# Optimization experiments

Hardware: AMD Instinct MI355X
Metric: run time of the kernel (lower is better)

## Reference

```python
import jax, jax.numpy as jnp
import numpy as np
from jax import lax

B, S, H, V, J, K = 8, 512, 768, 35004, 30, 9
PAD = 0

def setup_inputs() -> dict:
    key = jax.random.key(0)
    ks = jax.random.split(key, 12)
    std = 0.02
    return {
        'x': jax.random.randint(ks[0], (B, S), 0, V),
        'decoder_input': jax.random.normal(ks[1], (B, J, H), jnp.float32),
        'encoder_output': jax.random.normal(ks[2], (B, S, H), jnp.float32),
        'hidden': jax.random.normal(ks[3], (1, B, H), jnp.float32),
        'teacher': jax.random.randint(ks[4], (B, J, K), 0, V),
        'max_len': K,
        'embed': jax.random.normal(ks[5], (V, H), jnp.float32) * std,
        'w_ih': jax.random.normal(ks[6], (3 * H, H), jnp.float32) * std,
        'w_hh': jax.random.normal(ks[7], (3 * H, H), jnp.float32) * std,
        'b_ih': jnp.zeros((3 * H,), jnp.float32),
        'b_hh': jnp.zeros((3 * H,), jnp.float32),
        'wg_w': jax.random.normal(ks[8], (1, 3 * H), jnp.float32) * std,
        'wg_b': jnp.zeros((1,), jnp.float32),
    }

def gru_cell(w, h, w_ih, w_hh, b_ih, b_hh):
    # PyTorch GRU gate order: reset, update, new
    gi = w @ w_ih.T + b_ih          # [B,3H]
    gh = h @ w_hh.T + b_hh          # [B,3H]
    ir, iz, inn = jnp.split(gi, 3, axis=-1)
    hr, hz, hn = jnp.split(gh, 3, axis=-1)
    r = jax.nn.sigmoid(ir + hr)
    z = jax.nn.sigmoid(iz + hz)
    n = jnp.tanh(inn + r * hn)
    return (1.0 - z) * n + z * h

def reference(x, decoder_input, encoder_output, hidden, teacher, max_len,
              embed, w_ih, w_hh, b_ih, b_hh, wg_w, wg_b):
    mask = (x == PAD)                      # [B,S]
    batch_ix = jnp.arange(x.shape[0])[:, None]

    def tok_step(carry, teach_t):
        w, h = carry                       # w,h: [B,H]; teach_t: [B]
        h = gru_cell(w, h, w_ih, w_hh, b_ih, b_hh)
        logits_hist = jnp.einsum('bsh,bh->bs', encoder_output, h)
        logits_hist = jnp.where(mask, -1e9, logits_hist)
        a_hist = jax.nn.softmax(logits_hist, axis=-1)          # [B,S]
        a_vocab = jax.nn.softmax(h @ embed.T, axis=-1)         # [B,V]
        context = jnp.einsum('bs,bsh->bh', a_hist, encoder_output)
        p_gen = jax.nn.sigmoid(
            jnp.concatenate([w, h, context], axis=-1) @ wg_w.T + wg_b)  # [B,1]
        p_ctx = jnp.zeros_like(a_vocab).at[batch_ix, x].add(a_hist)     # scatter_add pointer copy
        p_final = p_gen * a_vocab + (1.0 - p_gen) * p_ctx
        w_next = embed[teach_t]            # teacher forcing (dropout omitted: eval mode)
        return (w_next, h), p_final

    def slot_step(h, slot_in):
        w0, teach_j = slot_in              # w0: [B,H]; teach_j: [K,B]
        (_, h), p = lax.scan(tok_step, (w0, h), teach_j)
        return h, p                        # p: [K,B,V]

    h0 = hidden[0]                                      # [B,H]
    slots = jnp.swapaxes(decoder_input, 0, 1)           # [J,B,H]
    teach = jnp.transpose(teacher, (1, 2, 0))           # [J,K,B]
    _, outs = lax.scan(slot_step, h0, (slots, teach))   # [J,K,B,V]
    return jnp.transpose(outs, (2, 0, 1, 3))            # [B,J,K,V]
```

## Files before the change

kernel.cpp:

```cpp
#include <hip/hip_runtime.h>
#include <hip/hip_bf16.h>

typedef _Float16 f16;
typedef _Float16 f16x8 __attribute__((ext_vector_type(8)));
typedef _Float16 h2 __attribute__((ext_vector_type(2)));
typedef float f32x4 __attribute__((ext_vector_type(4)));
typedef unsigned ui4v __attribute__((ext_vector_type(4)));
typedef unsigned long long ull;

#define B_ 8
#define S_ 512
#define H_ 768
#define V_ 35004
#define J_ 30
#define K_ 9
#define R_ 2160
#define H3 2304
#define CBLK 24
#define CUPB 32
#define VMT 17
#define VNT 274


__global__ void k_zero(int* p, int n) {
    int i = blockIdx.x * 256 + threadIdx.x;
    if (i < n) p[i] = 0;
}

__global__ void k_cast(const float* __restrict__ s, f16* __restrict__ d, long n) {
    for (long i = (long)blockIdx.x * 256 + threadIdx.x; i < n; i += (long)gridDim.x * 256)
        d[i] = (f16)s[i];
}

__global__ void k_build_wall(const float* __restrict__ emb, const float* __restrict__ dec,
                             const int* __restrict__ teacher, f16* __restrict__ Wall) {
    int r = blockIdx.x;
    int b = r / 270, s = r % 270, j = s / 9, t = s % 9;
    const float* src = (t == 0) ? dec + ((long)b * J_ + j) * H_
                                : emb + (long)teacher[((long)b * J_ + j) * K_ + (t - 1)] * H_;
    f16* dst = Wall + (long)r * H_;
    for (int c = threadIdx.x; c < H_; c += 256) dst[c] = (f16)src[c];
}

__global__ void k_build_enc(const float* __restrict__ enc, f16* __restrict__ ehi,
                            f16* __restrict__ elo, f16* __restrict__ encT) {
    long n = (long)B_ * S_ * H_;
    for (long i = (long)blockIdx.x * 256 + threadIdx.x; i < n; i += (long)gridDim.x * 256) {
        float v = enc[i];
        f16 hi = (f16)v;
        ehi[i] = hi;
        elo[i] = (f16)(v - (float)hi);
        int h = (int)(i % H_);
        long bs = i / H_;
        int s = (int)(bs % S_), b = (int)(bs / S_);
        encT[((long)b * H_ + h) * S_ + s] = hi;
    }
}

__global__ void k_init_h(const float* __restrict__ hidden, ull* __restrict__ hbuf) {
    int i = blockIdx.x * 256 + threadIdx.x;
    if (i < B_ * H_) {
        int b = i / H_, u = i % H_;
        hbuf[(long)b * 1536 + u] = (ull)__float_as_uint(hidden[i]);
    }
}

typedef const __attribute__((address_space(1))) unsigned GASU;
typedef __attribute__((address_space(3))) unsigned LASU;
__device__ __forceinline__ void gld16(const f16* g, f16* l) {
    __builtin_amdgcn_global_load_lds((GASU*)g, (LASU*)l, 16, 0, 0);
}

template <int MODE>
__global__ __launch_bounds__(256) void k_gemm(const f16* __restrict__ A, const f16* __restrict__ Bm,
                                              float* __restrict__ C, const float* __restrict__ bias,
                                              int M, int N, int K, long sA, long sB, long sC) {
    A += (long)blockIdx.z * sA;
    Bm += (long)blockIdx.z * sB;
    C += (long)blockIdx.z * sC;
    const int m0 = blockIdx.y * 128, n0 = blockIdx.x * 128;
    __shared__ f16 As[128 * 32];
    __shared__ f16 Bs[128 * 32];
    const int tid = threadIdx.x, lane = tid & 63, wave = tid >> 6;
    const int wm = wave >> 1, wn = wave & 1;
    const int fr = lane & 15, kg = lane >> 4;
    f32x4 acc[4][4] = {};
    const int idxu = wave * 128;
    const int i0 = idxu + lane, i1 = idxu + 64 + lane;
    const int r0 = i0 >> 2, k80 = i0 & 3;
    const int r1 = i1 >> 2, k81 = i1 & 3;
    int ga0 = m0 + r0; if (ga0 >= M) ga0 = M - 1;
    int ga1 = m0 + r1; if (ga1 >= M) ga1 = M - 1;
    int gb0 = n0 + r0; if (gb0 >= N) gb0 = N - 1;
    int gb1 = n0 + r1; if (gb1 >= N) gb1 = N - 1;
    const f16* pa0 = A + (long)ga0 * K + k80 * 8;
    const f16* pa1 = A + (long)ga1 * K + k81 * 8;
    const f16* pb0 = Bm + (long)gb0 * K + k80 * 8;
    const f16* pb1 = Bm + (long)gb1 * K + k81 * 8;
    for (int kt = 0; kt < K; kt += 32) {
        gld16(pa0 + kt, As + idxu * 8);
        gld16(pa1 + kt, As + idxu * 8 + 512);
        gld16(pb0 + kt, Bs + idxu * 8);
        gld16(pb1 + kt, Bs + idxu * 8 + 512);
        __syncthreads();
        f16x8 af[4], bf[4];
#pragma unroll
        for (int m = 0; m < 4; ++m) af[m] = *(const f16x8*)(As + (wm * 64 + m * 16 + fr) * 32 + kg * 8);
#pragma unroll
        for (int n = 0; n < 4; ++n) bf[n] = *(const f16x8*)(Bs + (wn * 64 + n * 16 + fr) * 32 + kg * 8);
#pragma unroll
        for (int m = 0; m < 4; ++m)
#pragma unroll
            for (int n = 0; n < 4; ++n)
                acc[m][n] = __builtin_amdgcn_mfma_f32_16x16x32_f16(af[m], bf[n], acc[m][n], 0, 0, 0);
        __syncthreads();
    }
    const int crow = m0 + wm * 64 + (lane >> 4) * 4;
    const int ccol = n0 + wn * 64 + fr;
#pragma unroll
    for (int n = 0; n < 4; ++n) {
        int col = ccol + n * 16;
        if (col >= N) continue;
        float bv = (MODE == 1) ? bias[col] : 0.f;
#pragma unroll
        for (int m = 0; m < 4; ++m) {
#pragma unroll
            for (int q = 0; q < 4; ++q) {
                int row = crow + m * 16 + q;
                if (row < M) C[(long)row * N + col] = acc[m][n][q] + bv;
            }
        }
    }
}

__global__ __launch_bounds__(256) void k_attn3(const f16* __restrict__ Ahi, const f16* __restrict__ Alo,
                                               const f16* __restrict__ Bhi, const f16* __restrict__ Blo,
                                               float* __restrict__ C, int M, int N, int K,
                                               long sA, long sB, long sC) {
    const long za = (long)blockIdx.z * sA, zb = (long)blockIdx.z * sB;
    C += (long)blockIdx.z * sC;
    const int m0 = blockIdx.y * 128, n0 = blockIdx.x * 128;
    __shared__ f16 As[128 * 32];
    __shared__ f16 Bs[128 * 32];
    const int tid = threadIdx.x, lane = tid & 63, wave = tid >> 6;
    const int wm = wave >> 1, wn = wave & 1;
    const int fr = lane & 15, kg = lane >> 4;
    f32x4 acc[4][4] = {};
    const int idxu = wave * 128;
    const int i0 = idxu + lane, i1 = idxu + 64 + lane;
    const int r0 = i0 >> 2, k80 = i0 & 3;
    const int r1 = i1 >> 2, k81 = i1 & 3;
    int ga0 = m0 + r0; if (ga0 >= M) ga0 = M - 1;
    int ga1 = m0 + r1; if (ga1 >= M) ga1 = M - 1;
    int gb0 = n0 + r0; if (gb0 >= N) gb0 = N - 1;
    int gb1 = n0 + r1; if (gb1 >= N) gb1 = N - 1;
    const long oa0 = (long)ga0 * K + k80 * 8, oa1 = (long)ga1 * K + k81 * 8;
    const long ob0 = (long)gb0 * K + k80 * 8, ob1 = (long)gb1 * K + k81 * 8;
    for (int ph = 0; ph < 3; ++ph) {
        const f16* Ap = (ph == 2 ? Alo : Ahi) + za;
        const f16* Bp = (ph == 1 ? Blo : Bhi) + zb;
        for (int kt = 0; kt < K; kt += 32) {
            gld16(Ap + oa0 + kt, As + idxu * 8);
            gld16(Ap + oa1 + kt, As + idxu * 8 + 512);
            gld16(Bp + ob0 + kt, Bs + idxu * 8);
            gld16(Bp + ob1 + kt, Bs + idxu * 8 + 512);
            __syncthreads();
            f16x8 af[4], bf[4];
#pragma unroll
            for (int m = 0; m < 4; ++m) af[m] = *(const f16x8*)(As + (wm * 64 + m * 16 + fr) * 32 + kg * 8);
#pragma unroll
            for (int n = 0; n < 4; ++n) bf[n] = *(const f16x8*)(Bs + (wn * 64 + n * 16 + fr) * 32 + kg * 8);
#pragma unroll
            for (int m = 0; m < 4; ++m)
#pragma unroll
                for (int n = 0; n < 4; ++n)
                    acc[m][n] = __builtin_amdgcn_mfma_f32_16x16x32_f16(af[m], bf[n], acc[m][n], 0, 0, 0);
            __syncthreads();
        }
    }
    const int crow = m0 + wm * 64 + (lane >> 4) * 4;
    const int ccol = n0 + wn * 64 + fr;
#pragma unroll
    for (int n = 0; n < 4; ++n) {
        int col = ccol + n * 16;
        if (col >= N) continue;
#pragma unroll
        for (int m = 0; m < 4; ++m) {
#pragma unroll
            for (int q = 0; q < 4; ++q) {
                int row = crow + m * 16 + q;
                if (row < M) C[(long)row * N + col] = acc[m][n][q];
            }
        }
    }
}

__global__ __launch_bounds__(256) void k_vocab(const f16* __restrict__ A, const f16* __restrict__ Bm,
                                               float* __restrict__ C, float* __restrict__ psum) {
    const int M = R_, N = V_, K = H_;
    const int nwg = VMT * VNT;
    int lin = blockIdx.x;
    int q8 = nwg / 8, r8 = nwg % 8;
    int xcd = lin & 7, idx = lin >> 3;
    int newlin = (xcd < r8) ? xcd * (q8 + 1) + idx : r8 * (q8 + 1) + (xcd - r8) * q8 + idx;
    int mt = newlin % VMT, nt = newlin / VMT;
    const int m0 = mt * 128, n0 = nt * 128;
    __shared__ f16 As[128 * 32];
    __shared__ f16 Bs[128 * 32];
    __shared__ float rpart[2][128];
    const int tid = threadIdx.x, lane = tid & 63, wave = tid >> 6;
    const int wm = wave >> 1, wn = wave & 1;
    const int fr = lane & 15, kg = lane >> 4;
    f32x4 acc[4][4] = {};
    const int idxu = wave * 128;
    const int i0 = idxu + lane, i1 = idxu + 64 + lane;
    const int r0 = i0 >> 2, k80 = i0 & 3;
    const int r1 = i1 >> 2, k81 = i1 & 3;
    int ga0 = m0 + r0; if (ga0 >= M) ga0 = M - 1;
    int ga1 = m0 + r1; if (ga1 >= M) ga1 = M - 1;
    int gb0 = n0 + r0; if (gb0 >= N) gb0 = N - 1;
    int gb1 = n0 + r1; if (gb1 >= N) gb1 = N - 1;
    const f16* pa0 = A + (long)ga0 * K + k80 * 8;
    const f16* pa1 = A + (long)ga1 * K + k81 * 8;
    const f16* pb0 = Bm + (long)gb0 * K + k80 * 8;
    const f16* pb1 = Bm + (long)gb1 * K + k81 * 8;
    for (int kt = 0; kt < K; kt += 32) {
        gld16(pa0 + kt, As + idxu * 8);
        gld16(pa1 + kt, As + idxu * 8 + 512);
        gld16(pb0 + kt, Bs + idxu * 8);
        gld16(pb1 + kt, Bs + idxu * 8 + 512);
        __syncthreads();
        f16x8 af[4], bf[4];
#pragma unroll
        for (int m = 0; m < 4; ++m) af[m] = *(const f16x8*)(As + (wm * 64 + m * 16 + fr) * 32 + kg * 8);
#pragma unroll
        for (int n = 0; n < 4; ++n) bf[n] = *(const f16x8*)(Bs + (wn * 64 + n * 16 + fr) * 32 + kg * 8);
#pragma unroll
        for (int m = 0; m < 4; ++m)
#pragma unroll
            for (int n = 0; n < 4; ++n)
                acc[m][n] = __builtin_amdgcn_mfma_f32_16x16x32_f16(af[m], bf[n], acc[m][n], 0, 0, 0);
        __syncthreads();
    }
    const int crow = m0 + wm * 64 + (lane >> 4) * 4;
    const int ccol = n0 + wn * 64 + fr;
    float rs[4][4];
#pragma unroll
    for (int m = 0; m < 4; ++m)
#pragma unroll
        for (int q = 0; q < 4; ++q) rs[m][q] = 0.f;
#pragma unroll
    for (int n = 0; n < 4; ++n) {
        int col = ccol + n * 16;
        if (col >= N) continue;
#pragma unroll
        for (int m = 0; m < 4; ++m) {
#pragma unroll
            for (int q = 0; q < 4; ++q) {
                int row = crow + m * 16 + q;
                if (row < M) {
                    float e = __expf(acc[m][n][q]);
                    C[(long)row * N + col] = e;
                    rs[m][q] += e;
                }
            }
        }
    }
#pragma unroll
    for (int m = 0; m < 4; ++m)
#pragma unroll
        for (int q = 0; q < 4; ++q) {
            float v = rs[m][q];
            v += __shfl_xor(v, 1);
            v += __shfl_xor(v, 2);
            v += __shfl_xor(v, 4);
            v += __shfl_xor(v, 8);
            rs[m][q] = v;
        }
    if ((lane & 15) == 0) {
#pragma unroll
        for (int m = 0; m < 4; ++m)
#pragma unroll
            for (int q = 0; q < 4; ++q)
                rpart[wn][wm * 64 + (lane >> 4) * 4 + m * 16 + q] = rs[m][q];
    }
    __syncthreads();
    if (tid < 128) {
        int row = m0 + tid;
        if (row < M) psum[(long)nt * M + row] = rpart[0][tid] + rpart[1][tid];
    }
}

__device__ __forceinline__ float fd2(unsigned hv, unsigned wv, float acc) {
#if __has_builtin(__builtin_amdgcn_fdot2)
    return __builtin_amdgcn_fdot2(__builtin_bit_cast(h2, hv), __builtin_bit_cast(h2, wv), acc, false);
#else
    h2 a = __builtin_bit_cast(h2, hv), b = __builtin_bit_cast(h2, wv);
    return acc + (float)a.x * (float)b.x + (float)a.y * (float)b.y;
#endif
}

__global__ __launch_bounds__(256, 1) void k_gru(const float* __restrict__ gi,
                                                const f16* __restrict__ wh16,
                                                const float* __restrict__ bhh,
                                                ull* hbuf,
                                                f16* __restrict__ Hhi, f16* __restrict__ Hlo) {
    __shared__ ui4v wsvu[9216];
    __shared__ __align__(16) f16 hsf[768];
    __shared__ float hs32[768];
    __shared__ float part[8][32][3];
    const int tid = threadIdx.x;
    const int chain = blockIdx.x / CBLK;
    const int blk = blockIdx.x % CBLK;
    const int u0 = blk * CUPB;
    for (int idx = tid; idx < 9216; idx += 256) {
        int uu = idx & 31, k8 = (idx >> 5) % 96, g = idx / (96 * 32);
        wsvu[idx] = *(const ui4v*)(wh16 + (long)(g * H_ + u0 + uu) * H_ + k8 * 8);
    }
    float b_r = 0.f, b_z = 0.f, b_n = 0.f;
    if (tid < 32) {
        int c = u0 + tid;
        b_r = bhh[c];
        b_z = bhh[H_ + c];
        b_n = bhh[2 * H_ + c];
    }
    __syncthreads();
    const int u = tid & 31, q = tid >> 5;
    ui4v wreg[3][12];
#pragma unroll
    for (int g = 0; g < 3; ++g)
#pragma unroll
        for (int i = 0; i < 12; ++i)
            wreg[g][i] = wsvu[(g * 96 + q * 12 + i) * 32 + u];
    ull* base = hbuf + (long)chain * 1536;
    for (int s = 0; s < 270; ++s) {
        const ull* rb = base + (s & 1) * 768;
        ull* wb = base + ((s + 1) & 1) * 768;
        const unsigned want = (unsigned)s;
        ull v0, v1, v2;
        for (;;) {
            v0 = __hip_atomic_load(rb + tid, __ATOMIC_RELAXED, __HIP_MEMORY_SCOPE_AGENT);
            v1 = __hip_atomic_load(rb + tid + 256, __ATOMIC_RELAXED, __HIP_MEMORY_SCOPE_AGENT);
            v2 = __hip_atomic_load(rb + tid + 512, __ATOMIC_RELAXED, __HIP_MEMORY_SCOPE_AGENT);
            bool ok = ((unsigned)(v0 >> 32) == want) & ((unsigned)(v1 >> 32) == want) &
                      ((unsigned)(v2 >> 32) == want);
            if (ok) break;
        }
        float f0 = __uint_as_float((unsigned)v0);
        float f1 = __uint_as_float((unsigned)v1);
        float f2 = __uint_as_float((unsigned)v2);
        hs32[tid] = f0;         hsf[tid] = (f16)f0;
        hs32[tid + 256] = f1;   hsf[tid + 256] = (f16)f1;
        hs32[tid + 512] = f2;   hsf[tid + 512] = (f16)f2;
        __syncthreads();
        float hold = 0.f, g0 = 0.f, g1 = 0.f, g2v = 0.f;
        if (tid < 32) {
            int c = u0 + tid;
            hold = hs32[c];
            const float* gp = gi + ((long)chain * 270 + s) * H3;
            g0 = gp[c];
            g1 = gp[H_ + c];
            g2v = gp[2 * H_ + c];
        }
        float ar = 0.f, az = 0.f, an = 0.f;
#pragma unroll
        for (int i = 0; i < 12; ++i) {
            ui4v hv = *(const ui4v*)(&hsf[(q * 12 + i) * 8]);
            ui4v wr = wreg[0][i], wz = wreg[1][i], wn = wreg[2][i];
            ar = fd2(hv.x, wr.x, ar); ar = fd2(hv.y, wr.y, ar);
            ar = fd2(hv.z, wr.z, ar); ar = fd2(hv.w, wr.w, ar);
            az = fd2(hv.x, wz.x, az); az = fd2(hv.y, wz.y, az);
            az = fd2(hv.z, wz.z, az); az = fd2(hv.w, wz.w, az);
            an = fd2(hv.x, wn.x, an); an = fd2(hv.y, wn.y, an);
            an = fd2(hv.z, wn.z, an); an = fd2(hv.w, wn.w, an);
        }
        part[q][u][0] = ar;
        part[q][u][1] = az;
        part[q][u][2] = an;
        __syncthreads();
        if (tid < 32) {
            float gr = b_r, gz = b_z, gn = b_n;
#pragma unroll
            for (int qq = 0; qq < 8; ++qq) {
                gr += part[qq][tid][0];
                gz += part[qq][tid][1];
                gn += part[qq][tid][2];
            }
            float rg = 1.f / (1.f + expf(-(g0 + gr)));
            float zg = 1.f / (1.f + expf(-(g1 + gz)));
            float ng = tanhf(g2v + rg * gn);
            float hnew = (1.f - zg) * ng + zg * hold;
            int c = u0 + tid;
            ull wv = ((ull)(unsigned)(s + 1) << 32) | (ull)__float_as_uint(hnew);
            __hip_atomic_store(wb + c, wv, __ATOMIC_RELAXED, __HIP_MEMORY_SCOPE_AGENT);
            long row = (long)chain * 270 + s;
            f16 hi16 = (f16)hnew;
            Hhi[row * H_ + c] = hi16;
            Hlo[row * H_ + c] = (f16)(hnew - (float)hi16);
        }
    }
}

__global__ __launch_bounds__(256) void k_attn_softmax(const float* __restrict__ lg,
                                                      const int* __restrict__ x, f16* __restrict__ ah) {
    __shared__ float red[256];
    int r = blockIdx.x, tid = threadIdx.x;
    int b = r / 270;
    const float* lr = lg + (long)r * S_;
    const int* xb = x + (long)b * S_;
    float v0 = lr[tid];
    if (xb[tid] == 0) v0 = -1e9f;
    float v1 = lr[tid + 256];
    if (xb[tid + 256] == 0) v1 = -1e9f;
    red[tid] = fmaxf(v0, v1);
    __syncthreads();
    for (int o = 128; o > 0; o >>= 1) {
        if (tid < o) red[tid] = fmaxf(red[tid], red[tid + o]);
        __syncthreads();
    }
    float m = red[0];
    __syncthreads();
    float e0 = __expf(v0 - m), e1 = __expf(v1 - m);
    red[tid] = e0 + e1;
    __syncthreads();
    for (int o = 128; o > 0; o >>= 1) {
        if (tid < o) red[tid] += red[tid + o];
        __syncthreads();
    }
    float inv = 1.f / red[0];
    ah[(long)r * S_ + tid] = (f16)(e0 * inv);
    ah[(long)r * S_ + tid + 256] = (f16)(e1 * inv);
}

__global__ __launch_bounds__(256) void k_pgen(const f16* __restrict__ Wall, const f16* __restrict__ Hhi,
                                              const f16* __restrict__ Hlo, const float* __restrict__ ctx,
                                              const float* __restrict__ wg, const float* __restrict__ wgb,
                                              float* __restrict__ pg) {
    __shared__ float red[256];
    int r = blockIdx.x, tid = threadIdx.x;
    float a = 0.f;
    for (int i = tid; i < H_; i += 256) {
        a += (float)Wall[(long)r * H_ + i] * wg[i];
        a += ((float)Hhi[(long)r * H_ + i] + (float)Hlo[(long)r * H_ + i]) * wg[H_ + i];
        a += ctx[(long)r * H_ + i] * wg[2 * H_ + i];
    }
    red[tid] = a;
    __syncthreads();
    for (int o = 128; o > 0; o >>= 1) {
        if (tid < o) red[tid] += red[tid + o];
        __syncthreads();
    }
    if (tid == 0) pg[r] = 1.f / (1.f + expf(-(red[0] + wgb[0])));
}

__global__ void k_redsum(const float* __restrict__ psum, float* __restrict__ rinv, int nb) {
    int r = blockIdx.x * 256 + threadIdx.x;
    if (r >= R_) return;
    float s = 0.f;
    for (int b = 0; b < nb; ++b) s += psum[(long)b * R_ + r];
    rinv[r] = 1.f / s;
}

__global__ __launch_bounds__(256) void k_final(float* __restrict__ out, const float* __restrict__ rinv,
                                               const float* __restrict__ pg) {
    int r = blockIdx.y;
    int i = blockIdx.x * 256 + threadIdx.x;
    if (i >= V_ / 4) return;
    float scale = pg[r] * rinv[r];
    f32x4* po = (f32x4*)(out + (long)r * V_);
    f32x4 v = po[i];
    v.x *= scale;
    v.y *= scale;
    v.z *= scale;
    v.w *= scale;
    po[i] = v;
}

__global__ __launch_bounds__(512) void k_scatter(float* __restrict__ out, const f16* __restrict__ ah,
                                                 const float* __restrict__ pg, const int* __restrict__ x) {
    int r = blockIdx.x, s = threadIdx.x;
    int b = r / 270;
    int xv = x[(long)b * S_ + s];
    if (xv == 0) return;
    float a = (float)ah[(long)r * S_ + s];
    if (a == 0.f) return;
    atomicAdd(out + (long)r * V_ + xv, (1.f - pg[r]) * a);
}

extern "C" void kernel_launch(void* const* d_in, const int* in_sizes, int n_in, void* d_out,
                              int out_size, void* d_ws, size_t ws_size, hipStream_t stream) {
    (void)in_sizes; (void)n_in; (void)out_size; (void)ws_size;
    const int* x = (const int*)d_in[0];
    const float* dec = (const float*)d_in[1];
    const float* enc = (const float*)d_in[2];
    const float* hid = (const float*)d_in[3];
    const int* tea = (const int*)d_in[4];
    const float* emb = (const float*)d_in[6];
    const float* wih = (const float*)d_in[7];
    const float* whh = (const float*)d_in[8];
    const float* bih = (const float*)d_in[9];
    const float* bhh = (const float*)d_in[10];
    const float* wgw = (const float*)d_in[11];
    const float* wgb = (const float*)d_in[12];
    float* out = (float*)d_out;

    char* w = (char*)d_ws;
    size_t off = 0;
    auto alloc = [&](size_t bytes) {
        void* p = w + off;
        off = (off + bytes + 255) & ~(size_t)255;
        return p;
    };
    ull* hbuf = (ull*)alloc(8 * 1536 * 8);
    f16* Wall = (f16*)alloc((size_t)R_ * H_ * 2);
    f16* wih16 = (f16*)alloc((size_t)H3 * H_ * 2);
    f16* wh16 = (f16*)alloc((size_t)H3 * H_ * 2);
    float* giA = (float*)alloc((size_t)R_ * H3 * 4);
    f16* Hhi = (f16*)alloc((size_t)R_ * H_ * 2);
    f16* Hlo = (f16*)alloc((size_t)R_ * H_ * 2);
    f16* emb16 = (f16*)alloc((size_t)V_ * H_ * 2);
    f16* ehi = (f16*)alloc((size_t)B_ * S_ * H_ * 2);
    f16* elo = (f16*)alloc((size_t)B_ * S_ * H_ * 2);
    f16* encT = (f16*)alloc((size_t)B_ * H_ * S_ * 2);
    float* lgH = (float*)alloc((size_t)R_ * S_ * 4);
    f16* ah = (f16*)alloc((size_t)R_ * S_ * 2);
    float* ctx = (float*)alloc((size_t)R_ * H_ * 4);
    float* pg = (float*)alloc(R_ * 4);
    float* psum = (float*)alloc((size_t)VNT * R_ * 4);
    float* rinv = (float*)alloc(R_ * 4);

    const int nH = 8 * 1536 * 2;
    k_zero<<<(nH + 255) / 256, 256, 0, stream>>>((int*)hbuf, nH);
    k_cast<<<2048, 256, 0, stream>>>(emb, emb16, (long)V_ * H_);
    k_cast<<<512, 256, 0, stream>>>(wih, wih16, (long)H3 * H_);
    k_cast<<<512, 256, 0, stream>>>(whh, wh16, (long)H3 * H_);
    k_build_wall<<<R_, 256, 0, stream>>>(emb, dec, tea, Wall);
    k_build_enc<<<1024, 256, 0, stream>>>(enc, ehi, elo, encT);
    k_init_h<<<24, 256, 0, stream>>>(hid, hbuf);

    {
        dim3 g(H3 / 128, (R_ + 127) / 128, 1);
        k_gemm<1><<<g, 256, 0, stream>>>(Wall, wih16, giA, bih, R_, H3, H_, 0, 0, 0);
    }
    k_gru<<<8 * CBLK, 256, 0, stream>>>(giA, wh16, bhh, hbuf, Hhi, Hlo);

    {
        dim3 g(S_ / 128, 3, 8);
        k_attn3<<<g, 256, 0, stream>>>(Hhi, Hlo, ehi, elo, lgH, 270, S_, H_,
                                       270L * H_, (long)S_ * H_, 270L * S_);
    }
    k_attn_softmax<<<R_, 256, 0, stream>>>(lgH, x, ah);
    {
        dim3 g(H_ / 128, 3, 8);
        k_gemm<0><<<g, 256, 0, stream>>>(ah, encT, ctx, nullptr, 270, H_, S_, 270L * S_, (long)H_ * S_, 270L * H_);
    }
    k_pgen<<<R_, 256, 0, stream>>>(Wall, Hhi, Hlo, ctx, wgw, wgb, pg);

    k_vocab<<<VMT * VNT, 256, 0, stream>>>(Hhi, emb16, out, psum);
    k_redsum<<<(R_ + 255) / 256, 256, 0, stream>>>(psum, rinv, VNT);
    {
        dim3 g((V_ / 4 + 255) / 256, R_, 1);
        k_final<<<g, 256, 0, stream>>>(out, rinv, pg);
    }
    k_scatter<<<R_, 512, 0, stream>>>(out, ah, pg, x);
}
```

Before: 1.152 ms.

## Overlap embedding/encoder casts with GRU recurrence in extra blocks, trim GRU sync

The embedding and encoder fp32-to-fp16 conversions move into 64 extra blocks of the persistent GRU kernel, so they run on otherwise idle CUs during the latency-bound recurrence instead of as separate launches. The W_hh cast is folded into the GRU's shared-memory load. Inside the step loop, each wave now polls only the hidden-state slice it writes into LDS, so one __syncthreads is replaced by a wave barrier. The old hidden value comes from a polled register, the next step's gate inputs are prefetched, and the partial-sum buffer is double-buffered. The extra blocks compete for memory bandwidth with the GRU spin-polling, and the design relies on all 256 blocks being co-resident.

```diff
diff --git a/kernel.cpp b/kernel.cpp
--- a/kernel.cpp
+++ b/kernel.cpp
@@ -3,6 +3,7 @@
 
 typedef _Float16 f16;
 typedef _Float16 f16x8 __attribute__((ext_vector_type(8)));
+typedef _Float16 f16x4v __attribute__((ext_vector_type(4)));
 typedef _Float16 h2 __attribute__((ext_vector_type(2)));
 typedef float f32x4 __attribute__((ext_vector_type(4)));
 typedef unsigned ui4v __attribute__((ext_vector_type(4)));
@@ -16,8 +17,6 @@
 #define K_ 9
 #define R_ 2160
 #define H3 2304
-#define CBLK 24
-#define CUPB 32
 #define VMT 17
 #define VNT 274
 
@@ -40,21 +39,6 @@
                                 : emb + (long)teacher[((long)b * J_ + j) * K_ + (t - 1)] * H_;
     f16* dst = Wall + (long)r * H_;
     for (int c = threadIdx.x; c < H_; c += 256) dst[c] = (f16)src[c];
-}
-
-__global__ void k_build_enc(const float* __restrict__ enc, f16* __restrict__ ehi,
-                            f16* __restrict__ elo, f16* __restrict__ encT) {
-    long n = (long)B_ * S_ * H_;
-    for (long i = (long)blockIdx.x * 256 + threadIdx.x; i < n; i += (long)gridDim.x * 256) {
-        float v = enc[i];
-        f16 hi = (f16)v;
-        ehi[i] = hi;
-        elo[i] = (f16)(v - (float)hi);
-        int h = (int)(i % H_);
-        long bs = i / H_;
-        int s = (int)(bs % S_), b = (int)(bs / S_);
-        encT[((long)b * H_ + h) * S_ + s] = hi;
-    }
 }
 
 __global__ void k_init_h(const float* __restrict__ hidden, ull* __restrict__ hbuf) {
@@ -301,21 +285,57 @@
 }
 
 __global__ __launch_bounds__(256, 1) void k_gru(const float* __restrict__ gi,
-                                                const f16* __restrict__ wh16,
+                                                const float* __restrict__ whh,
                                                 const float* __restrict__ bhh,
                                                 ull* hbuf,
-                                                f16* __restrict__ Hhi, f16* __restrict__ Hlo) {
+                                                f16* __restrict__ Hhi, f16* __restrict__ Hlo,
+                                                const float* __restrict__ emb, f16* __restrict__ emb16,
+                                                const float* __restrict__ enc, f16* __restrict__ ehi,
+                                                f16* __restrict__ elo, f16* __restrict__ encT) {
     __shared__ ui4v wsvu[9216];
     __shared__ __align__(16) f16 hsf[768];
-    __shared__ float hs32[768];
-    __shared__ float part[8][32][3];
+    __shared__ float part[2][8][32][3];
     const int tid = threadIdx.x;
-    const int chain = blockIdx.x / CBLK;
-    const int blk = blockIdx.x % CBLK;
-    const int u0 = blk * CUPB;
+    if (blockIdx.x >= 192) {
+        const long pt = (long)(blockIdx.x - 192) * 256 + tid;
+        const long n4 = (long)V_ * H_ / 4;
+        for (long i = pt; i < n4; i += 64 * 256) {
+            f32x4 v = ((const f32x4*)emb)[i];
+            f16x4v r = {(f16)v.x, (f16)v.y, (f16)v.z, (f16)v.w};
+            ((f16x4v*)emb16)[i] = r;
+        }
+        const long n4e = (long)B_ * S_ * H_ / 4;
+        for (long i = pt; i < n4e; i += 64 * 256) {
+            f32x4 v = ((const f32x4*)enc)[i];
+            long e0 = i * 4;
+            int h = (int)(e0 % H_);
+            long bs = e0 / H_;
+            int ss = (int)(bs % S_), bb = (int)(bs / S_);
+            f16 h0 = (f16)v.x, h1 = (f16)v.y, h2v = (f16)v.z, h3 = (f16)v.w;
+            f16x4v hv = {h0, h1, h2v, h3};
+            ((f16x4v*)ehi)[i] = hv;
+            f16x4v lv = {(f16)(v.x - (float)h0), (f16)(v.y - (float)h1),
+                         (f16)(v.z - (float)h2v), (f16)(v.w - (float)h3)};
+            ((f16x4v*)elo)[i] = lv;
+            f16* tp = encT + ((long)bb * H_ + h) * S_ + ss;
+            tp[0] = h0;
+            tp[S_] = h1;
+            tp[2L * S_] = h2v;
+            tp[3L * S_] = h3;
+        }
+        return;
+    }
+    const int chain = blockIdx.x / 24;
+    const int blk = blockIdx.x % 24;
+    const int u0 = blk * 32;
     for (int idx = tid; idx < 9216; idx += 256) {
         int uu = idx & 31, k8 = (idx >> 5) % 96, g = idx / (96 * 32);
-        wsvu[idx] = *(const ui4v*)(wh16 + (long)(g * H_ + u0 + uu) * H_ + k8 * 8);
+        const float* src = whh + (long)(g * H_ + u0 + uu) * H_ + k8 * 8;
+        f32x4 a = *(const f32x4*)src;
+        f32x4 b2 = *(const f32x4*)(src + 4);
+        f16x8 pk = {(f16)a.x, (f16)a.y, (f16)a.z, (f16)a.w,
+                    (f16)b2.x, (f16)b2.y, (f16)b2.z, (f16)b2.w};
+        wsvu[idx] = __builtin_bit_cast(ui4v, pk);
     }
     float b_r = 0.f, b_z = 0.f, b_n = 0.f;
     if (tid < 32) {
@@ -325,7 +345,8 @@
         b_n = bhh[2 * H_ + c];
     }
     __syncthreads();
-    const int u = tid & 31, q = tid >> 5;
+    const int u = tid & 31, q = tid >> 5, lane = tid & 63;
+    const int pw = (tid >> 6) * 192 + lane;
     ui4v wreg[3][12];
 #pragma unroll
     for (int g = 0; g < 3; ++g)
@@ -333,35 +354,36 @@
         for (int i = 0; i < 12; ++i)
             wreg[g][i] = wsvu[(g * 96 + q * 12 + i) * 32 + u];
     ull* base = hbuf + (long)chain * 1536;
+    const bool fin = (tid < 32);
+    float g0 = 0.f, g1 = 0.f, g2v = 0.f;
+    if (fin) {
+        const float* gp = gi + (long)chain * 270 * H3;
+        int c = u0 + tid;
+        g0 = gp[c];
+        g1 = gp[H_ + c];
+        g2v = gp[2 * H_ + c];
+    }
     for (int s = 0; s < 270; ++s) {
         const ull* rb = base + (s & 1) * 768;
         ull* wb = base + ((s + 1) & 1) * 768;
         const unsigned want = (unsigned)s;
-        ull v0, v1, v2;
+        ull v0, v1, v2, vh = 0;
         for (;;) {
-            v0 = __hip_atomic_load(rb + tid, __ATOMIC_RELAXED, __HIP_MEMORY_SCOPE_AGENT);
-            v1 = __hip_atomic_load(rb + tid + 256, __ATOMIC_RELAXED, __HIP_MEMORY_SCOPE_AGENT);
-            v2 = __hip_atomic_load(rb + tid + 512, __ATOMIC_RELAXED, __HIP_MEMORY_SCOPE_AGENT);
+            v0 = __hip_atomic_load(rb + pw, __ATOMIC_RELAXED, __HIP_MEMORY_SCOPE_AGENT);
+            v1 = __hip_atomic_load(rb + pw + 64, __ATOMIC_RELAXED, __HIP_MEMORY_SCOPE_AGENT);
+            v2 = __hip_atomic_load(rb + pw + 128, __ATOMIC_RELAXED, __HIP_MEMORY_SCOPE_AGENT);
             bool ok = ((unsigned)(v0 >> 32) == want) & ((unsigned)(v1 >> 32) == want) &
                       ((unsigned)(v2 >> 32) == want);
+            if (fin) {
+                vh = __hip_atomic_load(rb + u0 + tid, __ATOMIC_RELAXED, __HIP_MEMORY_SCOPE_AGENT);
+                ok &= ((unsigned)(vh >> 32) == want);
+            }
             if (ok) break;
         }
-        float f0 = __uint_as_float((unsigned)v0);
-        float f1 = __uint_as_float((unsigned)v1);
-        float f2 = __uint_as_float((unsigned)v2);
-        hs32[tid] = f0;         hsf[tid] = (f16)f0;
-        hs32[tid + 256] = f1;   hsf[tid + 256] = (f16)f1;
-        hs32[tid + 512] = f2;   hsf[tid + 512] = (f16)f2;
-        __syncthreads();
-        float hold = 0.f, g0 = 0.f, g1 = 0.f, g2v = 0.f;
-        if (tid < 32) {
-            int c = u0 + tid;
-            hold = hs32[c];
-            const float* gp = gi + ((long)chain * 270 + s) * H3;
-            g0 = gp[c];
-            g1 = gp[H_ + c];
-            g2v = gp[2 * H_ + c];
-        }
+        hsf[pw] = (f16)__uint_as_float((unsigned)v0);
+        hsf[pw + 64] = (f16)__uint_as_float((unsigned)v1);
+        hsf[pw + 128] = (f16)__uint_as_float((unsigned)v2);
+        __builtin_amdgcn_wave_barrier();
         float ar = 0.f, az = 0.f, an = 0.f;
 #pragma unroll
         for (int i = 0; i < 12; ++i) {
@@ -374,29 +396,37 @@
             an = fd2(hv.x, wn.x, an); an = fd2(hv.y, wn.y, an);
             an = fd2(hv.z, wn.z, an); an = fd2(hv.w, wn.w, an);
         }
-        part[q][u][0] = ar;
-        part[q][u][1] = az;
-        part[q][u][2] = an;
-        __syncthreads();
-        if (tid < 32) {
+        const int par = s & 1;
+        part[par][q][u][0] = ar;
+        part[par][q][u][1] = az;
+        part[par][q][u][2] = an;
+        __syncthreads();
+        if (fin) {
             float gr = b_r, gz = b_z, gn = b_n;
 #pragma unroll
             for (int qq = 0; qq < 8; ++qq) {
-                gr += part[qq][tid][0];
-                gz += part[qq][tid][1];
-                gn += part[qq][tid][2];
+                gr += part[par][qq][tid][0];
+                gz += part[par][qq][tid][1];
+                gn += part[par][qq][tid][2];
             }
+            float hold = __uint_as_float((unsigned)vh);
             float rg = 1.f / (1.f + expf(-(g0 + gr)));
             float zg = 1.f / (1.f + expf(-(g1 + gz)));
             float ng = tanhf(g2v + rg * gn);
             float hnew = (1.f - zg) * ng + zg * hold;
             int c = u0 + tid;
-            ull wv = ((ull)(unsigned)(s + 1) << 32) | (ull)__float_as_uint(hnew);
-            __hip_atomic_store(wb + c, wv, __ATOMIC_RELAXED, __HIP_MEMORY_SCOPE_AGENT);
+            ull wvv = ((ull)(unsigned)(s + 1) << 32) | (ull)__float_as_uint(hnew);
+            __hip_atomic_store(wb + c, wvv, __ATOMIC_RELAXED, __HIP_MEMORY_SCOPE_AGENT);
             long row = (long)chain * 270 + s;
-            f16 hi16 = (f16)hnew;
-            Hhi[row * H_ + c] = hi16;
-            Hlo[row * H_ + c] = (f16)(hnew - (float)hi16);
+            f16 h16 = (f16)hnew;
+            Hhi[row * H_ + c] = h16;
+            Hlo[row * H_ + c] = (f16)(hnew - (float)h16);
+            if (s < 269) {
+                const float* gp = gi + ((long)chain * 270 + s + 1) * H3;
+                g0 = gp[c];
+                g1 = gp[H_ + c];
+                g2v = gp[2 * H_ + c];
+            }
         }
     }
 }
@@ -514,7 +544,6 @@
     ull* hbuf = (ull*)alloc(8 * 1536 * 8);
     f16* Wall = (f16*)alloc((size_t)R_ * H_ * 2);
     f16* wih16 = (f16*)alloc((size_t)H3 * H_ * 2);
-    f16* wh16 = (f16*)alloc((size_t)H3 * H_ * 2);
     float* giA = (float*)alloc((size_t)R_ * H3 * 4);
     f16* Hhi = (f16*)alloc((size_t)R_ * H_ * 2);
     f16* Hlo = (f16*)alloc((size_t)R_ * H_ * 2);
@@ -531,18 +560,16 @@
 
     const int nH = 8 * 1536 * 2;
     k_zero<<<(nH + 255) / 256, 256, 0, stream>>>((int*)hbuf, nH);
-    k_cast<<<2048, 256, 0, stream>>>(emb, emb16, (long)V_ * H_);
     k_cast<<<512, 256, 0, stream>>>(wih, wih16, (long)H3 * H_);
-    k_cast<<<512, 256, 0, stream>>>(whh, wh16, (long)H3 * H_);
     k_build_wall<<<R_, 256, 0, stream>>>(emb, dec, tea, Wall);
-    k_build_enc<<<1024, 256, 0, stream>>>(enc, ehi, elo, encT);
     k_init_h<<<24, 256, 0, stream>>>(hid, hbuf);
 
     {
         dim3 g(H3 / 128, (R_ + 127) / 128, 1);
         k_gemm<1><<<g, 256, 0, stream>>>(Wall, wih16, giA, bih, R_, H3, H_, 0, 0, 0);
     }
-    k_gru<<<8 * CBLK, 256, 0, stream>>>(giA, wh16, bhh, hbuf, Hhi, Hlo);
+    k_gru<<<256, 256, 0, stream>>>(giA, whh, bhh, hbuf, Hhi, Hlo,
+                                   emb, emb16, enc, ehi, elo, encT);
 
     {
         dim3 g(S_ / 128, 3, 8);
```

After: 1.121 ms. -2.7%, faster.
